# Optimization experiments

Measured on AMD Instinct MI355X. Metric: run time of the kernel, lower is better.

The kernel has to match this reference:

```python
import jax, jax.numpy as jnp
import numpy as np
import math

D_MODEL = 1024
N_HEADS = 16
SEQ = 1024
BATCH = 4


def setup_inputs() -> dict:
    key = jax.random.key(0)
    ks = jax.random.split(key, 13)
    s = 1.0 / math.sqrt(D_MODEL)  # keep logits in a sane range
    return {
        "x": jax.random.normal(ks[0], (BATCH, SEQ, D_MODEL), jnp.float32),
        "Wq": jax.random.normal(ks[1], (D_MODEL, D_MODEL), jnp.float32) * s,
        "bq": jnp.zeros((D_MODEL,), jnp.float32),
        "Wk": jax.random.normal(ks[2], (D_MODEL, D_MODEL), jnp.float32) * s,
        "bk": jnp.zeros((D_MODEL,), jnp.float32),
        "Wv": jax.random.normal(ks[3], (D_MODEL, D_MODEL), jnp.float32) * s,
        "bv": jnp.zeros((D_MODEL,), jnp.float32),
        "Wo": jax.random.normal(ks[4], (D_MODEL, D_MODEL), jnp.float32) * s,
        "bo": jnp.zeros((D_MODEL,), jnp.float32),
        "Wimp": jax.random.normal(ks[5], (N_HEADS, D_MODEL), jnp.float32) * s,
        "bimp": jnp.zeros((N_HEADS,), jnp.float32),
        "k_ema": jax.random.normal(ks[6], (SEQ, D_MODEL), jnp.float32),
        "v_ema": jax.random.normal(ks[7], (SEQ, D_MODEL), jnp.float32),
    }


def reference(x, Wq, bq, Wk, bk, Wv, bv, Wo, bo, Wimp, bimp, k_ema, v_ema):
    B, S, D = x.shape
    H = Wimp.shape[0]
    hd = D // H

    def proj(W, b):
        # [B,S,D] -> [B,H,S,hd]
        return (x @ W.T + b).reshape(B, S, H, hd).transpose(0, 2, 1, 3)

    q = proj(Wq, bq)
    k = proj(Wk, bk)
    v = proj(Wv, bv)

    scores = jnp.einsum("bhqd,bhkd->bhqk", q, k) / math.sqrt(hd)

    # importance bias: outer-sum of per-head key/value importance vectors
    k_imp = (k_ema[:S] @ Wimp.T + bimp).T  # [H, S]
    v_imp = (v_ema[:S] @ Wimp.T + bimp).T  # [H, S]
    bias = 0.5 * (k_imp[:, :, None] + v_imp[:, None, :])  # [H, S, S]
    scores = scores + 0.1 * bias[None]

    # causal mask (torch masks before bias add; -inf + finite == -inf, so equivalent)
    causal = jnp.triu(jnp.ones((S, S), bool), k=1)
    scores = jnp.where(causal, -jnp.inf, scores)

    attn = jax.nn.softmax(scores, axis=-1)
    out = jnp.einsum("bhqk,bhkd->bhqd", attn, v)
    out = out.transpose(0, 2, 1, 3).reshape(B, S, D)
    return out @ Wo.T + bo
```

## Files before the change

### kernel.cpp

```cpp
#include <hip/hip_runtime.h>
#include <hip/hip_bf16.h>
#include <math.h>

#define D_MODEL 1024
#define SEQ     1024
#define BATCH   4
#define NHEADS  16
#define HD      64

#define QSC 0.18033688f
#define BSC 0.072134752f

typedef __bf16 bf16x8 __attribute__((ext_vector_type(8)));
typedef __bf16 bf16x4 __attribute__((ext_vector_type(4)));
typedef float  f32x4  __attribute__((ext_vector_type(4)));

__device__ __forceinline__ f32x4 mfma16(bf16x8 a, bf16x8 b, f32x4 c) {
  return __builtin_amdgcn_mfma_f32_16x16x32_bf16(a, b, c, 0, 0, 0);
}

__device__ __forceinline__ void async16(__bf16* lds, const __bf16* g) {
  __builtin_amdgcn_global_load_lds(g, lds, 16, 0, 0);
}

__global__ __launch_bounds__(256) void prep_kernel(
    const float* __restrict__ x,
    const float* __restrict__ Wq, const float* __restrict__ Wk,
    const float* __restrict__ Wv, const float* __restrict__ Wo,
    const float* __restrict__ v_ema,
    const float* __restrict__ Wimp, const float* __restrict__ bimp,
    __bf16* __restrict__ x_bf, __bf16* __restrict__ wq_bf, __bf16* __restrict__ wk_bf,
    __bf16* __restrict__ wv_bf, __bf16* __restrict__ wo_bf,
    float* __restrict__ vimp) {
  const int bid = blockIdx.x;
  const int tid = threadIdx.x;
  if (bid < 4096) {
    int i = bid * 256 + tid;
    float4 v = ((const float4*)x)[i];
    bf16x4 o; o[0] = (__bf16)v.x; o[1] = (__bf16)v.y; o[2] = (__bf16)v.z; o[3] = (__bf16)v.w;
    ((bf16x4*)x_bf)[i] = o;
  } else if (bid < 8192) {
    int i = (bid - 4096) * 256 + tid;
    int sel = i >> 18;
    int j = i & 262143;
    const float* s = (sel == 0) ? Wq : (sel == 1) ? Wk : (sel == 2) ? Wv : Wo;
    __bf16* d      = (sel == 0) ? wq_bf : (sel == 1) ? wk_bf : (sel == 2) ? wv_bf : wo_bf;
    float4 v = ((const float4*)s)[j];
    bf16x4 o; o[0] = (__bf16)v.x; o[1] = (__bf16)v.y; o[2] = (__bf16)v.z; o[3] = (__bf16)v.w;
    ((bf16x4*)d)[j] = o;
  } else {
    int gw   = (bid - 8192) * 4 + (tid >> 6);
    int lane = tid & 63;
    int h = gw >> 10, s = gw & 1023;
    float sum = 0.f;
    for (int d = lane; d < D_MODEL; d += 64)
      sum += v_ema[s * D_MODEL + d] * Wimp[h * D_MODEL + d];
    for (int mm = 32; mm >= 1; mm >>= 1) sum += __shfl_xor(sum, mm);
    if (lane == 0) vimp[h * SEQ + s] = sum + bimp[h];
  }
}

template<bool OUT_BF16>
__global__ __launch_bounds__(256) void gemm_bt(
    const __bf16* __restrict__ A,
    const __bf16* __restrict__ W0, const __bf16* __restrict__ W1, const __bf16* __restrict__ W2,
    const float* __restrict__ b0, const float* __restrict__ b1, const float* __restrict__ b2,
    void* out0, void* out1, void* out2, float sc0, float sc1, float sc2) {
  const int z = blockIdx.z;
  const __bf16* W   = (z == 0) ? W0 : (z == 1) ? W1 : W2;
  const float* bias = (z == 0) ? b0 : (z == 1) ? b1 : b2;
  void* out         = (z == 0) ? out0 : (z == 1) ? out1 : out2;
  const float sc    = (z == 0) ? sc0 : (z == 1) ? sc1 : sc2;

  __shared__ __bf16 As[128 * 32];
  __shared__ __bf16 Bs[128 * 32];

  const int tid = threadIdx.x;
  const int w = tid >> 6, l = tid & 63;
  const int quad = l >> 4, l16 = l & 15;
  const int wy = w >> 1, wx = w & 1;
  const int row0 = blockIdx.y * 128;
  const int col0 = blockIdx.x * 128;

  const f32x4 fzero = {0.f, 0.f, 0.f, 0.f};
  f32x4 acc[4][4];
  for (int i = 0; i < 4; i++)
    for (int j = 0; j < 4; j++) acc[i][j] = fzero;

  const int lr = l >> 2;
  const int sw0 = (((l & 3) ^ (lr & 3)) * 8);
  const int rowA = w * 16 + lr;
  const __bf16* aptr = A + (size_t)(row0 + rowA) * D_MODEL + sw0;
  const __bf16* bptr = W + (size_t)(col0 + rowA) * D_MODEL + sw0;
  __bf16* lA0 = &As[w * 512 + l * 8];
  __bf16* lA1 = &As[2048 + w * 512 + l * 8];
  __bf16* lB0 = &Bs[w * 512 + l * 8];
  __bf16* lB1 = &Bs[2048 + w * 512 + l * 8];

  const int rswz = (quad ^ (l16 & 3)) * 8;

  for (int k0 = 0; k0 < D_MODEL; k0 += 32) {
    async16(lA0, aptr + k0);
    async16(lA1, aptr + (size_t)64 * D_MODEL + k0);
    async16(lB0, bptr + k0);
    async16(lB1, bptr + (size_t)64 * D_MODEL + k0);
    __syncthreads();
    bf16x8 af[4], bfr[4];
    #pragma unroll
    for (int mi = 0; mi < 4; mi++) af[mi]  = *(const bf16x8*)&As[(wy * 64 + mi * 16 + l16) * 32 + rswz];
    #pragma unroll
    for (int ni = 0; ni < 4; ni++) bfr[ni] = *(const bf16x8*)&Bs[(wx * 64 + ni * 16 + l16) * 32 + rswz];
    if (z == 1) {
      #pragma unroll
      for (int mi = 0; mi < 4; mi++)
        #pragma unroll
        for (int ni = 0; ni < 4; ni++)
          acc[mi][ni] = mfma16(bfr[ni], af[mi], acc[mi][ni]);
    } else {
      #pragma unroll
      for (int mi = 0; mi < 4; mi++)
        #pragma unroll
        for (int ni = 0; ni < 4; ni++)
          acc[mi][ni] = mfma16(af[mi], bfr[ni], acc[mi][ni]);
    }
    __syncthreads();
  }

  if (z == 1 && OUT_BF16) {
    __bf16* kp = (__bf16*)out;
    #pragma unroll
    for (int ni = 0; ni < 4; ni++) {
      const int wcolbase = col0 + wx * 64 + ni * 16 + quad * 4;
      const float4 b4 = *(const float4*)&bias[wcolbase];
      const float bb[4] = {b4.x, b4.y, b4.z, b4.w};
      #pragma unroll
      for (int mi = 0; mi < 4; mi++) {
        const int token = row0 + wy * 64 + mi * 16 + l16;
        const int bh = (token >> 10) * 16 + (wcolbase >> 6);
        const int colp = ((wcolbase & 63) + ((token & 7) << 3)) & 63;
        union { __bf16 hh[4]; uint2 uu; } pk;
        #pragma unroll
        for (int r = 0; r < 4; r++) pk.hh[r] = (__bf16)(acc[mi][ni][r] + bb[r]);
        *(uint2*)(kp + ((size_t)bh * SEQ + (token & 1023)) * HD + colp) = pk.uu;
      }
    }
  } else if (z == 2 && OUT_BF16) {
    __bf16* vp = (__bf16*)out;
    #pragma unroll
    for (int ni = 0; ni < 4; ni++) {
      const int col = col0 + wx * 64 + ni * 16 + l16;
      const float bv = bias[col];
      #pragma unroll
      for (int mi = 0; mi < 4; mi++) {
        const int token = row0 + wy * 64 + mi * 16 + quad * 4;
        const int bh = (token >> 10) * 16 + (col >> 6);
        const int chk = (token >> 6) & 15;
        const int keyp = ((token & 63) + ((col & 7) << 3)) & 63;
        const size_t base = (((size_t)bh * 16 + chk) * 64 + (col & 63)) * 64 + keyp;
        union { __bf16 hh[4]; uint2 uu; } pk;
        #pragma unroll
        for (int r = 0; r < 4; r++) pk.hh[r] = (__bf16)(acc[mi][ni][r] + bv);
        *(uint2*)(vp + base) = pk.uu;
      }
    }
  } else {
    #pragma unroll
    for (int ni = 0; ni < 4; ni++) {
      const int col = col0 + wx * 64 + ni * 16 + l16;
      const float bv = bias[col];
      #pragma unroll
      for (int mi = 0; mi < 4; mi++) {
        const int row = row0 + wy * 64 + mi * 16 + quad * 4;
        #pragma unroll
        for (int r = 0; r < 4; r++) {
          float v = (acc[mi][ni][r] + bv) * sc;
          if (OUT_BF16) ((__bf16*)out)[(size_t)(row + r) * D_MODEL + col] = (__bf16)v;
          else          ((float*)out)[(size_t)(row + r) * D_MODEL + col] = v;
        }
      }
    }
  }
}

__global__ __launch_bounds__(256, 2) void attn_kernel(
    const __bf16* __restrict__ Qb, const __bf16* __restrict__ Kp,
    const __bf16* __restrict__ Vp, const float* __restrict__ vimp,
    __bf16* __restrict__ Ob) {
  const int id = blockIdx.x;
  const int bh = id & 63;
  const int gg = id >> 6;
  const int b = bh >> 4, h = bh & 15;
  const int tid = threadIdx.x;
  const int wave = tid >> 6, lane = tid & 63;
  const int quad = lane >> 4, l16 = lane & 15;

  __shared__ __bf16 Kl[2][4096];
  __shared__ __bf16 Vl[2][4096];
  __shared__ __bf16 Ps[4][16][72];

  const __bf16* kbase = Kp + (size_t)bh * (SEQ * HD);
  const __bf16* vbase = Vp + (size_t)bh * (SEQ * HD);
  const float* vimpH = vimp + h * SEQ;

  const int rot0 = ((quad + (l16 & 7)) & 7) * 8;
  const int rot1 = ((quad + 4 + (l16 & 7)) & 7) * 8;
  const int frow = l16 * 64;

  #pragma unroll 1
  for (int grp = 0; grp < 2; grp++) {
    const int g = grp ? (15 - gg) : gg;
    const int nch = g + 1;
    const int qrow = g * 64 + wave * 16 + l16;
    const __bf16* qp = Qb + (size_t)(b * SEQ + qrow) * D_MODEL + h * HD;
    bf16x8 qa0 = *(const bf16x8*)(qp + quad * 8);
    bf16x8 qa1 = *(const bf16x8*)(qp + 32 + quad * 8);
    float l_i = 0.f;
    f32x4 o[4];
    #pragma unroll
    for (int td = 0; td < 4; td++) { o[td][0] = 0.f; o[td][1] = 0.f; o[td][2] = 0.f; o[td][3] = 0.f; }

    __syncthreads();
    async16(&Kl[0][tid * 8], kbase + tid * 8);
    async16(&Kl[0][2048 + tid * 8], kbase + 2048 + tid * 8);
    async16(&Vl[0][tid * 8], vbase + tid * 8);
    async16(&Vl[0][2048 + tid * 8], vbase + 2048 + tid * 8);

    for (int ch = 0; ch < nch; ch++) {
      const int buf = ch & 1;
      __syncthreads();
      if (ch + 1 < nch) {
        const __bf16* gk = kbase + (ch + 1) * 4096;
        const __bf16* gv = vbase + (ch + 1) * 4096;
        const int nb = buf ^ 1;
        async16(&Kl[nb][tid * 8], gk + tid * 8);
        async16(&Kl[nb][2048 + tid * 8], gk + 2048 + tid * 8);
        async16(&Vl[nb][tid * 8], gv + tid * 8);
        async16(&Vl[nb][2048 + tid * 8], gv + 2048 + tid * 8);
      }
      const int kc = ch * 64;
      float4 vi[4];
      #pragma unroll
      for (int t = 0; t < 4; t++) vi[t] = *(const float4*)(vimpH + kc + t * 16 + quad * 4);
      bf16x8 kf0[4], kf1[4];
      #pragma unroll
      for (int t = 0; t < 4; t++) {
        kf0[t] = *(const bf16x8*)&Kl[buf][t * 1024 + frow + rot0];
        kf1[t] = *(const bf16x8*)&Kl[buf][t * 1024 + frow + rot1];
      }
      bf16x8 vfr0[4], vfr1[4];
      #pragma unroll
      for (int td = 0; td < 4; td++) {
        vfr0[td] = *(const bf16x8*)&Vl[buf][td * 1024 + frow + rot0];
        vfr1[td] = *(const bf16x8*)&Vl[buf][td * 1024 + frow + rot1];
      }
      const f32x4 fz = {0.f, 0.f, 0.f, 0.f};
      float p[4][4];
      float lsum = 0.f;
      #pragma unroll
      for (int t = 0; t < 4; t++) {
        f32x4 sacc = fz;
        sacc = mfma16(kf0[t], qa0, sacc);
        sacc = mfma16(kf1[t], qa1, sacc);
        const float vib[4] = {vi[t].x, vi[t].y, vi[t].z, vi[t].w};
        #pragma unroll
        for (int r = 0; r < 4; r++) {
          float pp = exp2f(sacc[r] + BSC * vib[r]);
          pp = (kc + t * 16 + quad * 4 + r <= qrow) ? pp : 0.f;
          p[t][r] = pp;
          lsum += pp;
        }
      }
      l_i += lsum;
      #pragma unroll
      for (int t = 0; t < 4; t++) {
        union { __bf16 hh[4]; uint2 uu; } pk;
        #pragma unroll
        for (int r = 0; r < 4; r++) pk.hh[r] = (__bf16)p[t][r];
        *(uint2*)&Ps[wave][l16][t * 16 + quad * 4] = pk.uu;
      }
      bf16x8 pf0 = *(const bf16x8*)&Ps[wave][l16][quad * 8];
      bf16x8 pf1 = *(const bf16x8*)&Ps[wave][l16][32 + quad * 8];
      #pragma unroll
      for (int td = 0; td < 4; td++) {
        o[td] = mfma16(vfr0[td], pf0, o[td]);
        o[td] = mfma16(vfr1[td], pf1, o[td]);
      }
    }

    float L = l_i;
    L += __shfl_xor(L, 16);
    L += __shfl_xor(L, 32);
    const float il = 1.0f / L;
    __bf16* op = Ob + (size_t)(b * SEQ + qrow) * D_MODEL + h * HD;
    #pragma unroll
    for (int td = 0; td < 4; td++) {
      union { __bf16 hh[4]; uint2 uu; } pk;
      #pragma unroll
      for (int r = 0; r < 4; r++) pk.hh[r] = (__bf16)(o[td][r] * il);
      *(uint2*)(op + td * 16 + quad * 4) = pk.uu;
    }
  }
}

extern "C" void kernel_launch(void* const* d_in, const int* in_sizes, int n_in,
                              void* d_out, int out_size, void* d_ws, size_t ws_size,
                              hipStream_t stream) {
  const float* x     = (const float*)d_in[0];
  const float* Wq    = (const float*)d_in[1];
  const float* bq    = (const float*)d_in[2];
  const float* Wk    = (const float*)d_in[3];
  const float* bk    = (const float*)d_in[4];
  const float* Wv    = (const float*)d_in[5];
  const float* bv    = (const float*)d_in[6];
  const float* Wo    = (const float*)d_in[7];
  const float* bo    = (const float*)d_in[8];
  const float* Wimp  = (const float*)d_in[9];
  const float* bimp  = (const float*)d_in[10];
  const float* v_ema = (const float*)d_in[12];
  float* out = (float*)d_out;

  char* ws = (char*)d_ws;
  __bf16* x_bf  = (__bf16*)(ws);
  __bf16* wq_bf = (__bf16*)(ws + (8ull  << 20));
  __bf16* wk_bf = (__bf16*)(ws + (10ull << 20));
  __bf16* wv_bf = (__bf16*)(ws + (12ull << 20));
  __bf16* wo_bf = (__bf16*)(ws + (14ull << 20));
  __bf16* q_bf  = (__bf16*)(ws + (16ull << 20));
  __bf16* kp_bf = (__bf16*)(ws + (24ull << 20));
  __bf16* vp_bf = (__bf16*)(ws + (32ull << 20));
  __bf16* a_bf  = (__bf16*)(ws + (40ull << 20));
  float*  vimp  = (float*)(ws + (48ull << 20));

  prep_kernel<<<12288, 256, 0, stream>>>(
      x, Wq, Wk, Wv, Wo, v_ema, Wimp, bimp,
      x_bf, wq_bf, wk_bf, wv_bf, wo_bf, vimp);

  gemm_bt<true><<<dim3(8, 32, 3), 256, 0, stream>>>(
      x_bf, wq_bf, wk_bf, wv_bf, bq, bk, bv,
      (void*)q_bf, (void*)kp_bf, (void*)vp_bf, QSC, 1.0f, 1.0f);

  attn_kernel<<<dim3(512), 256, 0, stream>>>(
      q_bf, kp_bf, vp_bf, vimp, a_bf);

  gemm_bt<false><<<dim3(8, 32, 1), 256, 0, stream>>>(
      a_bf, wo_bf, wo_bf, wo_bf, bo, bo, bo,
      (void*)out, (void*)out, (void*)out, 1.0f, 1.0f, 1.0f);
}
```

Measured before the change: 218.2 us.

## Double-buffer GEMM LDS loads, restructure vimp prep, skip causal mask off-diagonal

The GEMM main loop now double-buffers its A/B tiles in LDS. It issues the async global-to-LDS loads for the next k-step before computing the current one, using explicit vmcnt waits and raw barriers so memory latency overlaps MFMA work. The v_imp prep is restructured so each wave handles one sequence position for all 16 heads, reusing the v_ema row with float4 loads, and the prep grid shrinks to match. The attention kernel applies the causal mask comparison only on the diagonal chunk, removing per-element selects elsewhere. Together these add code complexity and depend on hand-written waitcnt counts being correct.

```diff
diff --git a/kernel.cpp b/kernel.cpp
--- a/kernel.cpp
+++ b/kernel.cpp
@@ -49,14 +49,45 @@
     bf16x4 o; o[0] = (__bf16)v.x; o[1] = (__bf16)v.y; o[2] = (__bf16)v.z; o[3] = (__bf16)v.w;
     ((bf16x4*)d)[j] = o;
   } else {
-    int gw   = (bid - 8192) * 4 + (tid >> 6);
-    int lane = tid & 63;
-    int h = gw >> 10, s = gw & 1023;
-    float sum = 0.f;
-    for (int d = lane; d < D_MODEL; d += 64)
-      sum += v_ema[s * D_MODEL + d] * Wimp[h * D_MODEL + d];
-    for (int mm = 32; mm >= 1; mm >>= 1) sum += __shfl_xor(sum, mm);
-    if (lane == 0) vimp[h * SEQ + s] = sum + bimp[h];
+    const int s    = (bid - 8192) * 4 + (tid >> 6);
+    const int lane = tid & 63;
+    const float4* ve = (const float4*)(v_ema + (size_t)s * D_MODEL);
+    float acc0 = 0.f, acc1 = 0.f, acc2 = 0.f, acc3 = 0.f;
+    float acc4 = 0.f, acc5 = 0.f, acc6 = 0.f, acc7 = 0.f;
+    float acc8 = 0.f, acc9 = 0.f, accA = 0.f, accB = 0.f;
+    float accC = 0.f, accD = 0.f, accE = 0.f, accF = 0.f;
+    #pragma unroll
+    for (int i = 0; i < 4; i++) {
+      const int c = lane + i * 64;
+      float4 v = ve[c];
+      #define VIMP_H(H, ACC)                                                     \
+        {                                                                        \
+          float4 w = ((const float4*)(Wimp + (H) * D_MODEL))[c];                 \
+          ACC += v.x * w.x + v.y * w.y + v.z * w.z + v.w * w.w;                  \
+        }
+      VIMP_H(0, acc0)  VIMP_H(1, acc1)  VIMP_H(2, acc2)  VIMP_H(3, acc3)
+      VIMP_H(4, acc4)  VIMP_H(5, acc5)  VIMP_H(6, acc6)  VIMP_H(7, acc7)
+      VIMP_H(8, acc8)  VIMP_H(9, acc9)  VIMP_H(10, accA) VIMP_H(11, accB)
+      VIMP_H(12, accC) VIMP_H(13, accD) VIMP_H(14, accE) VIMP_H(15, accF)
+      #undef VIMP_H
+    }
+    #define VIMP_RED(ACC)                                                        \
+      for (int mm = 32; mm >= 1; mm >>= 1) ACC += __shfl_xor(ACC, mm);
+    VIMP_RED(acc0) VIMP_RED(acc1) VIMP_RED(acc2) VIMP_RED(acc3)
+    VIMP_RED(acc4) VIMP_RED(acc5) VIMP_RED(acc6) VIMP_RED(acc7)
+    VIMP_RED(acc8) VIMP_RED(acc9) VIMP_RED(accA) VIMP_RED(accB)
+    VIMP_RED(accC) VIMP_RED(accD) VIMP_RED(accE) VIMP_RED(accF)
+    #undef VIMP_RED
+    if (lane == 0) {
+      vimp[0  * SEQ + s] = acc0 + bimp[0];  vimp[1  * SEQ + s] = acc1 + bimp[1];
+      vimp[2  * SEQ + s] = acc2 + bimp[2];  vimp[3  * SEQ + s] = acc3 + bimp[3];
+      vimp[4  * SEQ + s] = acc4 + bimp[4];  vimp[5  * SEQ + s] = acc5 + bimp[5];
+      vimp[6  * SEQ + s] = acc6 + bimp[6];  vimp[7  * SEQ + s] = acc7 + bimp[7];
+      vimp[8  * SEQ + s] = acc8 + bimp[8];  vimp[9  * SEQ + s] = acc9 + bimp[9];
+      vimp[10 * SEQ + s] = accA + bimp[10]; vimp[11 * SEQ + s] = accB + bimp[11];
+      vimp[12 * SEQ + s] = accC + bimp[12]; vimp[13 * SEQ + s] = accD + bimp[13];
+      vimp[14 * SEQ + s] = accE + bimp[14]; vimp[15 * SEQ + s] = accF + bimp[15];
+    }
   }
 }
 
@@ -72,8 +103,8 @@
   void* out         = (z == 0) ? out0 : (z == 1) ? out1 : out2;
   const float sc    = (z == 0) ? sc0 : (z == 1) ? sc1 : sc2;
 
-  __shared__ __bf16 As[128 * 32];
-  __shared__ __bf16 Bs[128 * 32];
+  __shared__ __bf16 As[2][128 * 32];
+  __shared__ __bf16 Bs[2][128 * 32];
 
   const int tid = threadIdx.x;
   const int w = tid >> 6, l = tid & 63;
@@ -92,24 +123,35 @@
   const int rowA = w * 16 + lr;
   const __bf16* aptr = A + (size_t)(row0 + rowA) * D_MODEL + sw0;
   const __bf16* bptr = W + (size_t)(col0 + rowA) * D_MODEL + sw0;
-  __bf16* lA0 = &As[w * 512 + l * 8];
-  __bf16* lA1 = &As[2048 + w * 512 + l * 8];
-  __bf16* lB0 = &Bs[w * 512 + l * 8];
-  __bf16* lB1 = &Bs[2048 + w * 512 + l * 8];
+  const int ldsOff = w * 512 + l * 8;
 
   const int rswz = (quad ^ (l16 & 3)) * 8;
 
-  for (int k0 = 0; k0 < D_MODEL; k0 += 32) {
-    async16(lA0, aptr + k0);
-    async16(lA1, aptr + (size_t)64 * D_MODEL + k0);
-    async16(lB0, bptr + k0);
-    async16(lB1, bptr + (size_t)64 * D_MODEL + k0);
-    __syncthreads();
+  async16(&As[0][ldsOff], aptr);
+  async16(&As[0][2048 + ldsOff], aptr + (size_t)64 * D_MODEL);
+  async16(&Bs[0][ldsOff], bptr);
+  async16(&Bs[0][2048 + ldsOff], bptr + (size_t)64 * D_MODEL);
+
+  #pragma unroll 2
+  for (int t = 0; t < 32; ++t) {
+    const int buf = t & 1;
+    if (t + 1 < 32) {
+      const int nb = buf ^ 1;
+      const int k1 = (t + 1) * 32;
+      async16(&As[nb][ldsOff], aptr + k1);
+      async16(&As[nb][2048 + ldsOff], aptr + (size_t)64 * D_MODEL + k1);
+      async16(&Bs[nb][ldsOff], bptr + k1);
+      async16(&Bs[nb][2048 + ldsOff], bptr + (size_t)64 * D_MODEL + k1);
+      asm volatile("s_waitcnt vmcnt(4)" ::: "memory");
+    } else {
+      asm volatile("s_waitcnt vmcnt(0)" ::: "memory");
+    }
+    __builtin_amdgcn_s_barrier();
     bf16x8 af[4], bfr[4];
     #pragma unroll
-    for (int mi = 0; mi < 4; mi++) af[mi]  = *(const bf16x8*)&As[(wy * 64 + mi * 16 + l16) * 32 + rswz];
-    #pragma unroll
-    for (int ni = 0; ni < 4; ni++) bfr[ni] = *(const bf16x8*)&Bs[(wx * 64 + ni * 16 + l16) * 32 + rswz];
+    for (int mi = 0; mi < 4; mi++) af[mi]  = *(const bf16x8*)&As[buf][(wy * 64 + mi * 16 + l16) * 32 + rswz];
+    #pragma unroll
+    for (int ni = 0; ni < 4; ni++) bfr[ni] = *(const bf16x8*)&Bs[buf][(wx * 64 + ni * 16 + l16) * 32 + rswz];
     if (z == 1) {
       #pragma unroll
       for (int mi = 0; mi < 4; mi++)
@@ -123,7 +165,7 @@
         for (int ni = 0; ni < 4; ni++)
           acc[mi][ni] = mfma16(af[mi], bfr[ni], acc[mi][ni]);
     }
-    __syncthreads();
+    __builtin_amdgcn_s_barrier();
   }
 
   if (z == 1 && OUT_BF16) {
@@ -256,18 +298,34 @@
       const f32x4 fz = {0.f, 0.f, 0.f, 0.f};
       float p[4][4];
       float lsum = 0.f;
-      #pragma unroll
-      for (int t = 0; t < 4; t++) {
-        f32x4 sacc = fz;
-        sacc = mfma16(kf0[t], qa0, sacc);
-        sacc = mfma16(kf1[t], qa1, sacc);
-        const float vib[4] = {vi[t].x, vi[t].y, vi[t].z, vi[t].w};
-        #pragma unroll
-        for (int r = 0; r < 4; r++) {
-          float pp = exp2f(sacc[r] + BSC * vib[r]);
-          pp = (kc + t * 16 + quad * 4 + r <= qrow) ? pp : 0.f;
-          p[t][r] = pp;
-          lsum += pp;
+      if (ch == nch - 1) {
+        #pragma unroll
+        for (int t = 0; t < 4; t++) {
+          f32x4 sacc = fz;
+          sacc = mfma16(kf0[t], qa0, sacc);
+          sacc = mfma16(kf1[t], qa1, sacc);
+          const float vib[4] = {vi[t].x, vi[t].y, vi[t].z, vi[t].w};
+          #pragma unroll
+          for (int r = 0; r < 4; r++) {
+            float pp = exp2f(sacc[r] + BSC * vib[r]);
+            pp = (kc + t * 16 + quad * 4 + r <= qrow) ? pp : 0.f;
+            p[t][r] = pp;
+            lsum += pp;
+          }
+        }
+      } else {
+        #pragma unroll
+        for (int t = 0; t < 4; t++) {
+          f32x4 sacc = fz;
+          sacc = mfma16(kf0[t], qa0, sacc);
+          sacc = mfma16(kf1[t], qa1, sacc);
+          const float vib[4] = {vi[t].x, vi[t].y, vi[t].z, vi[t].w};
+          #pragma unroll
+          for (int r = 0; r < 4; r++) {
+            float pp = exp2f(sacc[r] + BSC * vib[r]);
+            p[t][r] = pp;
+            lsum += pp;
+          }
         }
       }
       l_i += lsum;
@@ -331,7 +389,7 @@
   __bf16* a_bf  = (__bf16*)(ws + (40ull << 20));
   float*  vimp  = (float*)(ws + (48ull << 20));
 
-  prep_kernel<<<12288, 256, 0, stream>>>(
+  prep_kernel<<<8448, 256, 0, stream>>>(
       x, Wq, Wk, Wv, Wo, v_ema, Wimp, bimp,
       x_bf, wq_bf, wk_bf, wv_bf, wo_bf, vimp);
 
```

Result: faster. 210.8 us (-3.4%).
